# Kernel tuning notes

Measured on AMD Instinct MI355X. Metric: run time of the kernel, lower is better.

Reference implementation:

```python
import jax, jax.numpy as jnp
import numpy as np

SR = 16000
FLEN = 400        # round(winlen * samplerate)
STEP = 160        # round(winstep * samplerate)
NFFT = 512
NFILT = 26
NUMCEP = 13
PREEMPH = 0.97
CEPLIFTER = 22
LOWFREQ = 0.0
HIGHFREQ = SR / 2.0
EPS = float(np.finfo(np.float32).eps)


def _hz2mel(hz):
    return 2595.0 * np.log10(1.0 + hz / 700.0)


def _mel2hz(mel):
    return 700.0 * (10.0 ** (mel / 2595.0) - 1.0)


def _filterbanks():
    # [NFFT//2+1, NFILT] mel triangular filterbank (transposed, as used in torch.mm)
    melpoints = np.linspace(_hz2mel(LOWFREQ), _hz2mel(HIGHFREQ), NFILT + 2)
    bins = np.floor((NFFT + 1) * _mel2hz(melpoints) / SR)
    fb = np.zeros([NFILT, NFFT // 2 + 1], dtype=np.float64)
    for j in range(NFILT):
        for i in range(int(bins[j]), int(bins[j + 1])):
            fb[j, i] = (i - bins[j]) / (bins[j + 1] - bins[j])
        for i in range(int(bins[j + 1]), int(bins[j + 2])):
            fb[j, i] = (bins[j + 2] - i) / (bins[j + 2] - bins[j + 1])
    return fb.T  # [257, 26]


def _dct_mat(N, k):
    # orthonormal DCT-II matrix rows 0..k-1: [k, N]
    n = np.arange(N)
    kk = np.arange(k)[:, None]
    C = np.cos(np.pi * (2 * n[None, :] + 1) * kk / (2.0 * N))
    C[0] *= 1.0 / np.sqrt(N)
    C[1:] *= np.sqrt(2.0 / N)
    return C


def setup_inputs() -> dict:
    key = jax.random.key(0)
    k1, k2 = jax.random.split(key)
    signals = jax.random.normal(k1, (64, 320000), dtype=jnp.float32)
    lengths = jax.random.randint(k2, (64,), 0, 320000, dtype=jnp.int32)
    return {"signals": signals, "lengths": lengths}


def reference(signals, lengths):
    B, T = signals.shape
    F = 1 if T <= FLEN else 1 + int(np.ceil((T - FLEN) / float(STEP)))
    padlen = (F - 1) * STEP + FLEN

    # preemphasis (uses self.preemph=0.97), masked past each sample's length
    pre = jnp.concatenate(
        [signals[:, :1], signals[:, 1:] - PREEMPH * signals[:, :-1]], axis=1)
    pos = jnp.arange(T)
    pre = jnp.where(pos[None, :] < lengths[:, None], pre, jnp.zeros((), pre.dtype))

    # framing: [B, F, FLEN]
    pad = jnp.pad(pre, ((0, 0), (0, padlen - T)))
    idx = np.arange(FLEN)[None, :] + STEP * np.arange(F)[:, None]
    frames = pad[:, idx]

    # power spectrum, [B, F, NFFT//2+1]
    spec = jnp.fft.rfft(frames, n=NFFT, axis=-1)
    pspec = (spec.real * spec.real + spec.imag * spec.imag) / NFFT
    energy = pspec.sum(-1) + EPS                      # [B, F]

    fb = jnp.asarray(_filterbanks(), dtype=signals.dtype)     # [257, 26]
    feat = jnp.log(pspec @ fb + EPS)                  # [B, F, 26]

    dctm = jnp.asarray(_dct_mat(NFILT, NUMCEP), dtype=signals.dtype)  # [13, 26]
    ceps = jnp.einsum('bfn,kn->bfk', feat, dctm)      # [B, F, 13]

    n = jnp.arange(NUMCEP, dtype=signals.dtype)
    lift = 1.0 + (CEPLIFTER / 2.0) * jnp.sin(np.pi * n / CEPLIFTER)
    ceps = ceps * lift
    ceps = ceps.at[:, :, 0].set(jnp.log(energy))       # appendEnergy

    # per-sample number of frames; zero-pad rest (original pads to batch max)
    nframes = jnp.where(
        lengths <= FLEN, 1,
        1 + jnp.ceil((lengths - FLEN) / float(STEP)).astype(jnp.int32))
    fmask = jnp.arange(F)[None, :] < nframes[:, None]
    ceps = jnp.where(fmask[:, :, None], ceps, jnp.zeros((), ceps.dtype))
    return ceps, nframes
```

## Files before the change

kernel.cpp:

```cpp
#include <hip/hip_runtime.h>
#include <math.h>

#define SRATE   16000
#define FLEN    400
#define STEP    160
#define NFFT    512
#define NBINS   257
#define NFILT   26
#define NUMCEP  13
#define BATCH   64
#define TLEN    320000
#define NFRAMES 1999
#define NGRP    500
#define EPSF    1.1920929e-07f
#define PI_F    3.14159265358979323846f

typedef float    v2f __attribute__((ext_vector_type(2)));
typedef unsigned uv2 __attribute__((ext_vector_type(2)));

__device__ __forceinline__ v2f mk2(float a, float b) { v2f v; v.x = a; v.y = b; return v; }
__device__ __forceinline__ v2f pfma(v2f a, v2f b, v2f c) { return __builtin_elementwise_fma(a, b, c); }

template<int CTRL>
__device__ __forceinline__ float fdpp(float x) {
    return __builtin_bit_cast(float, __builtin_amdgcn_mov_dpp(
        __builtin_bit_cast(int, x), CTRL, 0xF, 0xF, true));
}
template<int IMM>
__device__ __forceinline__ float fswz(float x) {
    return __builtin_bit_cast(float, __builtin_amdgcn_ds_swizzle(
        __builtin_bit_cast(int, x), IMM));
}
__device__ __forceinline__ uv2 pl32(float x) {
    unsigned u = __builtin_bit_cast(unsigned, x);
    return __builtin_amdgcn_permlane32_swap(u, u, false, false);
}
__device__ __forceinline__ float fxor32(float x, bool hi32) {
    uv2 r = pl32(x);
    return __builtin_bit_cast(float, hi32 ? r[0] : r[1]);
}
#define DPP_X1   0xB1
#define DPP_X2   0x4E
#define DPP_X8   0x128
#define SWZ_X4   0x101F
#define SWZ_X16  0x401F

__global__ void mfcc_setup_kernel(const int* __restrict__ lengths,
                                  void* __restrict__ ws,
                                  float* __restrict__ out_nframes) {
    int tid = threadIdx.x;
    int*   bins = (int*)ws;
    float* dctw = (float*)ws + 32;

    if (tid < 28) {
        double M    = 2595.0 * log10(1.0 + 8000.0 / 700.0);
        double step = M / 27.0;
        double mel  = (tid == 27) ? M : (double)tid * step;
        double hz   = 700.0 * (pow(10.0, mel / 2595.0) - 1.0);
        bins[tid] = (int)floor((double)(NFFT + 1) * hz / (double)SRATE);
    }
    for (int t = tid; t < NUMCEP * NFILT; t += 64) {
        int k = t / NFILT, j = t - k * NFILT;
        double v = cos(M_PI * (double)((2 * j + 1) * k) / (2.0 * (double)NFILT));
        v *= (k == 0) ? 1.0 / sqrt((double)NFILT) : sqrt(2.0 / (double)NFILT);
        double lift = 1.0 + 11.0 * sin(M_PI * (double)k / 22.0);
        dctw[t] = (float)(v * lift);
    }
    if (tid < BATCH) {
        int len = lengths[tid];
        int nf  = (len <= FLEN) ? 1 : 1 + (len - FLEN + STEP - 1) / STEP;
        out_nframes[tid] = (float)nf;
    }
}

__launch_bounds__(256, 2)
__global__ void mfcc_kernel(const float* __restrict__ sig,
                            const int*   __restrict__ lengths,
                            const void*  __restrict__ ws,
                            float*       __restrict__ out) {
    __shared__ v2f psA[4][260];
    __shared__ v2f psB[4][260];
    __shared__ v2f featAs[4][28], featBs[4][28];
    __shared__ float dctS[NUMCEP * NFILT];
    __shared__ int   binsS[NFILT + 2];

    const int tid  = threadIdx.x;
    const int lane = tid & 63;
    const int w    = tid >> 6;

    {
        const int*   binsG = (const int*)ws;
        const float* dctG  = (const float*)ws + 32;
        for (int t = tid; t < NUMCEP * NFILT; t += 256) dctS[t] = dctG[t];
        if (tid < NFILT + 2) binsS[tid] = binsG[tid];
    }
    __syncthreads();

    const int G  = blockIdx.x * 4 + w;
    const int b  = G / NGRP;
    const int q  = G - b * NGRP;
    const int f0 = 4 * q;
    const int len = lengths[b];
    const int nf  = (len <= FLEN) ? 1 : 1 + (len - FLEN + STEP - 1) / STEP;

    if (f0 >= nf) {
        if (lane < 52) {
            int d13 = lane / 13;
            int kk  = lane - 13 * d13;
            int ff  = f0 + d13;
            if (ff < NFRAMES)
                out[((long)b * NFRAMES + ff) * NUMCEP + kk] = 0.0f;
        }
        return;
    }

    const float* s = sig + (long)b * TLEN;
    const int base = f0 * STEP;

    const int B   = (int)(__brev((unsigned)lane) >> 26);
    const int i0  = 8 * B;
    const bool liveB = (i0 < FLEN);

    v2f Zr0[4], Zi0[4], Zr1[4], Zi1[4];
    const bool fastw = (base >= 1) && (base + 880 <= len);
    if (fastw) {
        float w0[9], w1[9], w2[9], w3[9];
        if (liveB) {
            const float4* sv = (const float4*)(s + base + i0);
            float4 a0 = sv[-1],  a1 = sv[0],   a2 = sv[1];
            float4 b0 = sv[39],  b1 = sv[40],  b2 = sv[41];
            float4 c0 = sv[79],  c1 = sv[80],  c2 = sv[81];
            float4 d0 = sv[119], d1 = sv[120], d2 = sv[121];
#define UNPK(W, q0, q1, q2)                                                   \
            W[0] = q0.w; W[1] = q1.x; W[2] = q1.y; W[3] = q1.z; W[4] = q1.w;  \
            W[5] = q2.x; W[6] = q2.y; W[7] = q2.z; W[8] = q2.w;
            UNPK(w0, a0, a1, a2)
            UNPK(w1, b0, b1, b2)
            UNPK(w2, c0, c1, c2)
            UNPK(w3, d0, d1, d2)
#undef UNPK
        } else {
            #pragma unroll
            for (int j = 0; j < 9; ++j) { w0[j] = w1[j] = w2[j] = w3[j] = 0.0f; }
        }
        #pragma unroll
        for (int m = 0; m < 4; ++m) {
            const int j = (m == 0) ? 0 : (m == 1) ? 4 : (m == 2) ? 2 : 6;
            Zr0[m] = mk2(fmaf(-0.97f, w0[j],     w0[j + 1]),
                         fmaf(-0.97f, w0[j + 1], w0[j + 2]));
            Zi0[m] = mk2(fmaf(-0.97f, w1[j],     w1[j + 1]),
                         fmaf(-0.97f, w1[j + 1], w1[j + 2]));
            Zr1[m] = mk2(fmaf(-0.97f, w2[j],     w2[j + 1]),
                         fmaf(-0.97f, w2[j + 1], w2[j + 2]));
            Zi1[m] = mk2(fmaf(-0.97f, w3[j],     w3[j + 1]),
                         fmaf(-0.97f, w3[j + 1], w3[j + 2]));
        }
    } else {
        float w0[9], w1[9], w2[9], w3[9];
        const int tb0 = base + i0 - 1;
        #pragma unroll
        for (int j = 0; j < 9; ++j) {
            int t0 = tb0 + j;
            w0[j] = (liveB && t0 >= 0 && t0 < len) ? s[t0] : 0.0f;
            int t1 = t0 + 160; w1[j] = (liveB && t1 < len) ? s[t1] : 0.0f;
            int t2 = t0 + 320; w2[j] = (liveB && t2 < len) ? s[t2] : 0.0f;
            int t3 = t0 + 480; w3[j] = (liveB && t3 < len) ? s[t3] : 0.0f;
        }
        const int tbe = base + i0;
        #pragma unroll
        for (int m = 0; m < 4; ++m) {
            const int j = (m == 0) ? 0 : (m == 1) ? 4 : (m == 2) ? 2 : 6;
#define ASMW(Wk, OFF, DST)                                                    \
            { float va = fmaf(-0.97f, Wk[j],     Wk[j + 1]);                  \
              float vb = fmaf(-0.97f, Wk[j + 1], Wk[j + 2]);                  \
              bool ma = liveB && (tbe + (OFF) + j)     < len;                 \
              bool mb = liveB && (tbe + (OFF) + j + 1) < len;                 \
              DST = mk2(ma ? va : 0.0f, mb ? vb : 0.0f); }
            ASMW(w0, 0,   Zr0[m])
            ASMW(w1, 160, Zi0[m])
            ASMW(w2, 320, Zr1[m])
            ASMW(w3, 480, Zi1[m])
#undef ASMW
        }
    }

    const float ang = -PI_F * (float)lane / 256.0f;
    float T1i = __sinf(ang);
    float T1r = __cosf(ang);
#define SQC(orr, oii, ir, ii) { float _r = ir * ir - ii * ii; oii = 2.0f * ir * ii; orr = _r; }
    float T2r, T2i;   SQC(T2r, T2i, T1r, T1i)
    float T4r, T4i;   SQC(T4r, T4i, T2r, T2i)
    float T8r, T8i;   SQC(T8r, T8i, T4r, T4i)
    float T16r, T16i; SQC(T16r, T16i, T8r, T8i)
    float T32r, T32i; SQC(T32r, T32i, T16r, T16i)
    float T64r, T64i; SQC(T64r, T64i, T32r, T32i)
    float T128r, T128i; SQC(T128r, T128i, T64r, T64i)
    const float RH = 0.70710678118654752f;
    const float A1r = RH * (T1r + T1i), A1i = RH * (T1i - T1r);
    const float A2r = T1i,              A2i = -T1r;
    const float A3r = RH * (T1i - T1r), A3i = -RH * (T1r + T1i);

    {
        const float sg = (lane & 1) ? -1.0f : 1.0f;
        const v2f sg2 = mk2(sg, sg);
        #pragma unroll
        for (int m = 0; m < 4; ++m) {
            v2f pr0 = mk2(fdpp<DPP_X1>(Zr0[m].x), fdpp<DPP_X1>(Zr0[m].y));
            v2f pi0 = mk2(fdpp<DPP_X1>(Zi0[m].x), fdpp<DPP_X1>(Zi0[m].y));
            v2f pr1 = mk2(fdpp<DPP_X1>(Zr1[m].x), fdpp<DPP_X1>(Zr1[m].y));
            v2f pi1 = mk2(fdpp<DPP_X1>(Zi1[m].x), fdpp<DPP_X1>(Zi1[m].y));
            Zr0[m] = pfma(sg2, Zr0[m], pr0);
            Zi0[m] = pfma(sg2, Zi0[m], pi0);
            Zr1[m] = pfma(sg2, Zr1[m], pr1);
            Zi1[m] = pfma(sg2, Zi1[m], pi1);
        }
    }

#define PK_XSTAGE2(d, UR, UI, SH)                                             \
    {                                                                         \
        const bool hi_ = (lane & (d)) != 0;                                   \
        const float ur = hi_ ? (UR) : 1.0f;                                   \
        const float ui = hi_ ? (UI) : 0.0f;                                   \
        const float sg = hi_ ? 1.0f : -1.0f;                                  \
        const v2f ur2 = mk2(ur, ur), ui2 = mk2(ui, ui);                       \
        const v2f nui2 = mk2(-ui, -ui), sg2 = mk2(sg, sg);                    \
        _Pragma("unroll")                                                     \
        for (int m = 0; m < 4; ++m) {                                         \
            v2f tr0 = pfma(Zi0[m], nui2, Zr0[m] * ur2);                       \
            v2f ti0 = pfma(Zi0[m], ur2,  Zr0[m] * ui2);                       \
            v2f tr1 = pfma(Zi1[m], nui2, Zr1[m] * ur2);                       \
            v2f ti1 = pfma(Zi1[m], ur2,  Zr1[m] * ui2);                       \
            v2f pr0 = mk2(SH(tr0.x), SH(tr0.y));                              \
            v2f pi0 = mk2(SH(ti0.x), SH(ti0.y));                              \
            v2f pr1 = mk2(SH(tr1.x), SH(tr1.y));                              \
            v2f pi1 = mk2(SH(ti1.x), SH(ti1.y));                              \
            Zr0[m] = pfma(sg2, pr0, tr0);                                     \
            Zi0[m] = pfma(sg2, pi0, ti0);                                     \
            Zr1[m] = pfma(sg2, pr1, tr1);                                     \
            Zi1[m] = pfma(sg2, pi1, ti1);                                     \
        }                                                                     \
    }
#define SH_X2(v)  fdpp<DPP_X2>(v)
#define SH_X4(v)  fswz<SWZ_X4>(v)
#define SH_X8(v)  fdpp<DPP_X8>(v)
#define SH_X16(v) fswz<SWZ_X16>(v)
#define SH_X32(v) fxor32(v, hi_)
    PK_XSTAGE2(2,  T128r, T128i, SH_X2)
    PK_XSTAGE2(4,  T64r,  T64i,  SH_X4)
    PK_XSTAGE2(8,  T32r,  T32i,  SH_X8)
    PK_XSTAGE2(16, T16r,  T16i,  SH_X16)
    PK_XSTAGE2(32, T8r,   T8i,   SH_X32)

#define PBFLY2(A, Bv, WR, WI)                                                 \
    {                                                                         \
        const v2f wr2 = mk2((WR), (WR)), wi2 = mk2((WI), (WI));               \
        const v2f nwi2 = mk2(-(WI), -(WI));                                   \
        v2f tr0 = pfma(Zi0[Bv], nwi2, Zr0[Bv] * wr2);                         \
        v2f ti0 = pfma(Zi0[Bv], wr2,  Zr0[Bv] * wi2);                         \
        v2f tr1 = pfma(Zi1[Bv], nwi2, Zr1[Bv] * wr2);                         \
        v2f ti1 = pfma(Zi1[Bv], wr2,  Zr1[Bv] * wi2);                         \
        Zr0[Bv] = Zr0[A] - tr0;  Zi0[Bv] = Zi0[A] - ti0;                      \
        Zr0[A]  = Zr0[A] + tr0;  Zi0[A]  = Zi0[A] + ti0;                      \
        Zr1[Bv] = Zr1[A] - tr1;  Zi1[Bv] = Zi1[A] - ti1;                      \
        Zr1[A]  = Zr1[A] + tr1;  Zi1[A]  = Zi1[A] + ti1;                      \
    }
    PBFLY2(0, 1, T4r, T4i)
    PBFLY2(2, 3, T4r, T4i)
    PBFLY2(0, 2, T2r, T2i)
    PBFLY2(1, 3, T2i, -T2r)

    float zrA[8], ziA[8], zrB[8], ziB[8];
    #pragma unroll
    for (int m = 0; m < 4; ++m) {
        const float Wr = (m == 0) ? T1r : (m == 1) ? A1r : (m == 2) ? A2r : A3r;
        const float Wi = (m == 0) ? T1i : (m == 1) ? A1i : (m == 2) ? A2i : A3i;
        { float tr = Zr0[m].y * Wr - Zi0[m].y * Wi;
          float ti = Zr0[m].y * Wi + Zi0[m].y * Wr;
          zrA[m]     = Zr0[m].x + tr;  ziA[m]     = Zi0[m].x + ti;
          zrA[m + 4] = Zr0[m].x - tr;  ziA[m + 4] = Zi0[m].x - ti; }
        { float tr = Zr1[m].y * Wr - Zi1[m].y * Wi;
          float ti = Zr1[m].y * Wi + Zi1[m].y * Wr;
          zrB[m]     = Zr1[m].x + tr;  ziB[m]     = Zi1[m].x + ti;
          zrB[m + 4] = Zr1[m].x - tr;  ziB[m + 4] = Zi1[m].x - ti; }
    }

    v2f* PA = psA[w];
    v2f* PB = psB[w];
    const float inv = 1.0f / (4.0f * (float)NFFT);
    v2f eA = mk2(0.0f, 0.0f), eB = mk2(0.0f, 0.0f);
    const int ml = (64 - lane) & 63;
    #pragma unroll
    for (int r = 0; r < 4; ++r) {
        float mrA = __shfl(zrA[7 - r], ml), miA = __shfl(ziA[7 - r], ml);
        float mrB = __shfl(zrB[7 - r], ml), miB = __shfl(ziB[7 - r], ml);
        if (lane == 0) {
            mrA = zrA[(8 - r) & 7]; miA = ziA[(8 - r) & 7];
            mrB = zrB[(8 - r) & 7]; miB = ziB[(8 - r) & 7];
        }
        { float ar = zrA[r] + mrA, ai = ziA[r] - miA;
          float br = ziA[r] + miA, bi = zrA[r] - mrA;
          v2f p = mk2((ar * ar + ai * ai) * inv, (br * br + bi * bi) * inv);
          PA[64 * r + lane] = p;  eA += p; }
        { float ar = zrB[r] + mrB, ai = ziB[r] - miB;
          float br = ziB[r] + miB, bi = zrB[r] - mrB;
          v2f p = mk2((ar * ar + ai * ai) * inv, (br * br + bi * bi) * inv);
          PB[64 * r + lane] = p;  eB += p; }
    }
    if (lane == 0) {
        v2f pA = mk2(4.0f * zrA[4] * zrA[4] * inv, 4.0f * ziA[4] * ziA[4] * inv);
        v2f pB = mk2(4.0f * zrB[4] * zrB[4] * inv, 4.0f * ziB[4] * ziB[4] * inv);
        PA[256] = pA;  eA += pA;
        PB[256] = pB;  eB += pB;
    }
#define ERED(E)                                                               \
    E = E + mk2(fdpp<DPP_X1>(E.x),  fdpp<DPP_X1>(E.y));                       \
    E = E + mk2(fdpp<DPP_X2>(E.x),  fdpp<DPP_X2>(E.y));                       \
    E = E + mk2(fswz<SWZ_X4>(E.x),  fswz<SWZ_X4>(E.y));                       \
    E = E + mk2(fdpp<DPP_X8>(E.x),  fdpp<DPP_X8>(E.y));                       \
    E = E + mk2(fswz<SWZ_X16>(E.x), fswz<SWZ_X16>(E.y));                      \
    { uv2 rx = pl32(E.x), ry = pl32(E.y);                                     \
      E = mk2(__builtin_bit_cast(float, rx[0]) + __builtin_bit_cast(float, rx[1]), \
              __builtin_bit_cast(float, ry[0]) + __builtin_bit_cast(float, ry[1])); }
    ERED(eA)
    ERED(eB)
    __builtin_amdgcn_wave_barrier();

    const int  j  = lane & 31;
    const bool hi = lane >= 32;
    {
        const v2f* P = hi ? PB : PA;
        v2f fu = mk2(0, 0), fs = mk2(0, 0), fu2 = mk2(0, 0), fs2 = mk2(0, 0);
        if (j <= NFILT) {
            int bA = binsS[j], bZ = binsS[j + 1];
            int i = bA;
            for (; i + 1 < bZ; i += 2) {
                v2f p = P[i], p2 = P[i + 1];
                float c0 = (float)(i - bA), c1 = (float)(i + 1 - bA);
                fs  += p;   fu  = pfma(p,  mk2(c0, c0), fu);
                fs2 += p2;  fu2 = pfma(p2, mk2(c1, c1), fu2);
            }
            if (i < bZ) {
                v2f p = P[i];
                float c0 = (float)(i - bA);
                fs += p;  fu = pfma(p, mk2(c0, c0), fu);
            }
            fs += fs2;  fu += fu2;
            float iw = (bZ > bA) ? 1.0f / (float)(bZ - bA) : 0.0f;
            fu = fu * mk2(iw, iw);
        }
        v2f down = fs - fu;
        v2f dn = mk2(__shfl(down.x, lane + 1), __shfl(down.y, lane + 1));
        if (j < NFILT) {
            v2f ft = fu + dn;
            v2f fv = mk2(__logf(ft.x + EPSF), __logf(ft.y + EPSF));
            if (hi) featBs[w][j] = fv; else featAs[w][j] = fv;
        }
    }
    __builtin_amdgcn_wave_barrier();

    if (j < NUMCEP) {
        const v2f* ft = hi ? featBs[w] : featAs[w];
        v2f a0 = mk2(0, 0), a1 = mk2(0, 0);
        #pragma unroll
        for (int jj = 0; jj < NFILT; jj += 2) {
            float c0 = dctS[j * NFILT + jj], c1 = dctS[j * NFILT + jj + 1];
            a0 = pfma(ft[jj],     mk2(c0, c0), a0);
            a1 = pfma(ft[jj + 1], mk2(c1, c1), a1);
        }
        v2f val = a0 + a1;
        if (j == 0) {
            v2f E = hi ? eB : eA;
            val = mk2(__logf(E.x + EPSF), __logf(E.y + EPSF));
        }
        const int fb = f0 + (hi ? 2 : 0);
        long o0 = ((long)b * NFRAMES + fb) * NUMCEP + j;
        if (fb < NFRAMES)     out[o0]          = (fb     >= nf) ? 0.0f : val.x;
        if (fb + 1 < NFRAMES) out[o0 + NUMCEP] = (fb + 1 >= nf) ? 0.0f : val.y;
    }
}

extern "C" void kernel_launch(void* const* d_in, const int* in_sizes, int n_in,
                              void* d_out, int out_size, void* d_ws, size_t ws_size,
                              hipStream_t stream) {
    const float* sig     = (const float*)d_in[0];
    const int*   lengths = (const int*)d_in[1];
    float* out = (float*)d_out;

    mfcc_setup_kernel<<<1, 64, 0, stream>>>(lengths, d_ws,
                                            out + (size_t)BATCH * NFRAMES * NUMCEP);

    const int total_groups = BATCH * NGRP;
    mfcc_kernel<<<total_groups / 4, 256, 0, stream>>>(sig, lengths, d_ws, out);
}
```

Measured before the change: 51.79 us.

## Compact frame groups via prefix-sum over live frames and zero output separately

```diff
diff --git a/kernel.cpp b/kernel.cpp
--- a/kernel.cpp
+++ b/kernel.cpp
@@ -11,9 +11,10 @@
 #define BATCH   64
 #define TLEN    320000
 #define NFRAMES 1999
-#define NGRP    500
 #define EPSF    1.1920929e-07f
 #define PI_F    3.14159265358979323846f
+
+#define CEPS_N  (BATCH * NFRAMES * NUMCEP)
 
 typedef float    v2f __attribute__((ext_vector_type(2)));
 typedef unsigned uv2 __attribute__((ext_vector_type(2)));
@@ -39,18 +40,33 @@
     uv2 r = pl32(x);
     return __builtin_bit_cast(float, hi32 ? r[0] : r[1]);
 }
+#if __has_builtin(__builtin_amdgcn_permlane16_swap)
+__device__ __forceinline__ float fxor16(float x, bool hi16) {
+    unsigned u = __builtin_bit_cast(unsigned, x);
+    uv2 r = __builtin_amdgcn_permlane16_swap(u, u, false, false);
+    return __builtin_bit_cast(float, hi16 ? r[0] : r[1]);
+}
+#define SH_X16(v) fxor16(v, hi_)
+#else
+#define SH_X16(v) fswz<0x401F>(v)
+#endif
+
 #define DPP_X1   0xB1
 #define DPP_X2   0x4E
 #define DPP_X8   0x128
 #define SWZ_X4   0x101F
 #define SWZ_X16  0x401F
 
+#define WS_DCT  32
+#define WS_QOFF 370
+
 __global__ void mfcc_setup_kernel(const int* __restrict__ lengths,
                                   void* __restrict__ ws,
                                   float* __restrict__ out_nframes) {
     int tid = threadIdx.x;
     int*   bins = (int*)ws;
-    float* dctw = (float*)ws + 32;
+    float* dctw = (float*)ws + WS_DCT;
+    int*   qoff = (int*)ws + WS_QOFF;
 
     if (tid < 28) {
         double M    = 2595.0 * log10(1.0 + 8000.0 / 700.0);
@@ -66,11 +82,24 @@
         double lift = 1.0 + 11.0 * sin(M_PI * (double)k / 22.0);
         dctw[t] = (float)(v * lift);
     }
-    if (tid < BATCH) {
+    {
         int len = lengths[tid];
         int nf  = (len <= FLEN) ? 1 : 1 + (len - FLEN + STEP - 1) / STEP;
         out_nframes[tid] = (float)nf;
-    }
+        int x = (nf + 3) >> 2;
+        #pragma unroll
+        for (int off = 1; off < 64; off <<= 1) {
+            int y = __shfl_up(x, off);
+            if (tid >= off) x += y;
+        }
+        qoff[tid + 1] = x;
+        if (tid == 0) qoff[0] = 0;
+    }
+}
+
+__global__ void mfcc_zero_kernel(float4* __restrict__ p) {
+    int i = blockIdx.x * blockDim.x + threadIdx.x;
+    if (i < CEPS_N / 4) p[i] = float4{0.0f, 0.0f, 0.0f, 0.0f};
 }
 
 __launch_bounds__(256, 2)
@@ -88,31 +117,27 @@
     const int lane = tid & 63;
     const int w    = tid >> 6;
 
+    const int* qoffG = (const int*)ws + WS_QOFF;
+    const int total = qoffG[64];
+    if ((int)blockIdx.x * 4 >= total) return;
+
     {
         const int*   binsG = (const int*)ws;
-        const float* dctG  = (const float*)ws + 32;
+        const float* dctG  = (const float*)ws + WS_DCT;
         for (int t = tid; t < NUMCEP * NFILT; t += 256) dctS[t] = dctG[t];
         if (tid < NFILT + 2) binsS[tid] = binsG[tid];
     }
     __syncthreads();
 
-    const int G  = blockIdx.x * 4 + w;
-    const int b  = G / NGRP;
-    const int q  = G - b * NGRP;
+    const int L = blockIdx.x * 4 + w;
+    if (L >= total) return;
+    int qv = qoffG[lane];
+    unsigned long long mm = __ballot(qv <= L);
+    const int b  = __popcll(mm) - 1;
+    const int q  = L - qoffG[b];
     const int f0 = 4 * q;
     const int len = lengths[b];
     const int nf  = (len <= FLEN) ? 1 : 1 + (len - FLEN + STEP - 1) / STEP;
-
-    if (f0 >= nf) {
-        if (lane < 52) {
-            int d13 = lane / 13;
-            int kk  = lane - 13 * d13;
-            int ff  = f0 + d13;
-            if (ff < NFRAMES)
-                out[((long)b * NFRAMES + ff) * NUMCEP + kk] = 0.0f;
-        }
-        return;
-    }
 
     const float* s = sig + (long)b * TLEN;
     const int base = f0 * STEP;
@@ -243,7 +268,6 @@
 #define SH_X2(v)  fdpp<DPP_X2>(v)
 #define SH_X4(v)  fswz<SWZ_X4>(v)
 #define SH_X8(v)  fdpp<DPP_X8>(v)
-#define SH_X16(v) fswz<SWZ_X16>(v)
 #define SH_X32(v) fxor32(v, hi_)
     PK_XSTAGE2(2,  T128r, T128i, SH_X2)
     PK_XSTAGE2(4,  T64r,  T64i,  SH_X4)
@@ -374,8 +398,8 @@
         }
         const int fb = f0 + (hi ? 2 : 0);
         long o0 = ((long)b * NFRAMES + fb) * NUMCEP + j;
-        if (fb < NFRAMES)     out[o0]          = (fb     >= nf) ? 0.0f : val.x;
-        if (fb + 1 < NFRAMES) out[o0 + NUMCEP] = (fb + 1 >= nf) ? 0.0f : val.y;
+        if (fb < nf)     out[o0]          = val.x;
+        if (fb + 1 < nf) out[o0 + NUMCEP] = val.y;
     }
 }
 
@@ -386,9 +410,8 @@
     const int*   lengths = (const int*)d_in[1];
     float* out = (float*)d_out;
 
-    mfcc_setup_kernel<<<1, 64, 0, stream>>>(lengths, d_ws,
-                                            out + (size_t)BATCH * NFRAMES * NUMCEP);
-
-    const int total_groups = BATCH * NGRP;
-    mfcc_kernel<<<total_groups / 4, 256, 0, stream>>>(sig, lengths, d_ws, out);
-}
+    mfcc_zero_kernel<<<(CEPS_N / 4 + 255) / 256, 256, 0, stream>>>((float4*)out);
+    mfcc_setup_kernel<<<1, 64, 0, stream>>>(lengths, d_ws, out + (size_t)CEPS_N);
+
+    mfcc_kernel<<<8000, 256, 0, stream>>>(sig, lengths, d_ws, out);
+}
```

New measurement: 54.99 us. +6.2%, slower.
